# Kernel optimization log

Hardware: AMD Instinct MI355X
Metric: run time of the kernel (lower is better)

Reference implementation:

```python
import jax, jax.numpy as jnp
import numpy as np

IN_FEATURES = 4096
OUT_FEATURES = 11008
GROUP_SIZE = 32
M_TOKENS = 32
Q_MID = 8  # int4 midpoint: dequant = (q - 8) * scale + zero


def setup_inputs() -> dict:
    key = jax.random.key(0)
    k1, k2, k3, k4 = jax.random.split(key, 4)
    n_groups = IN_FEATURES // GROUP_SIZE
    inputs = {
        "input": jax.random.normal(k1, (M_TOKENS, IN_FEATURES), dtype=jnp.float32),
        "weight": jax.random.randint(k2, (OUT_FEATURES, IN_FEATURES), 0, 16, dtype=jnp.int32),
        "scales_and_zeros": jax.random.normal(k3, (n_groups, OUT_FEATURES, 2), dtype=jnp.float32),
        "bias": jax.random.normal(k4, (OUT_FEATURES,), dtype=jnp.float32),
        "group_size": GROUP_SIZE,
    }
    return inputs


def reference(input, weight, scales_and_zeros, bias, group_size):
    out_features, in_features = weight.shape
    n_groups = in_features // group_size
    # scales/zeros per (group, out) -> [out, n_groups]
    scale = scales_and_zeros[..., 0].T  # [out, G]
    zero = scales_and_zeros[..., 1].T   # [out, G]
    # dequantize int4 weight: w = (q - 8) * scale + zero, per group along in_features
    q = weight.astype(jnp.float32).reshape(out_features, n_groups, group_size)
    w_fp = (q - Q_MID) * scale[:, :, None] + zero[:, :, None]  # [out, G, gs]
    w_fp = w_fp.reshape(out_features, in_features)
    # y = x @ W^T + b
    y = jnp.einsum("bi,oi->bo", input, w_fp) + bias
    return y
```

## Files before the change

kernel.cpp:

```cpp
#include <hip/hip_runtime.h>
#include <hip/hip_bf16.h>
#include <stdint.h>

#define M_TOK 32
#define IN_F 4096
#define OUT_F 11008
#define NSPLIT 4
#define KRANGE (IN_F / NSPLIT)
#define KC 128
#define NTILE 64
#define LDA 136
#define LDB 136

typedef __attribute__((ext_vector_type(8))) short bf16x8;
typedef __attribute__((ext_vector_type(4))) float f32x4;

__device__ inline uint32_t pack_bf16(float a, float b) {
    __hip_bfloat16 ha = __float2bfloat16(a);
    __hip_bfloat16 hb = __float2bfloat16(b);
    uint16_t ua = *(uint16_t*)&ha;
    uint16_t ub = *(uint16_t*)&hb;
    return (uint32_t)ua | ((uint32_t)ub << 16);
}

__global__ void init_out_kernel(const float* __restrict__ bias, float* __restrict__ out) {
    int o = blockIdx.x * 256 + threadIdx.x;
    int m = blockIdx.y;
    out[(size_t)m * OUT_F + o] = bias[o];
}

__launch_bounds__(256)
__global__ void qgemm_kernel(const float* __restrict__ x,
                             const int* __restrict__ wq,
                             const float* __restrict__ sz,
                             float* __restrict__ out) {
    __shared__ __align__(16) short A[M_TOK * LDA];
    __shared__ __align__(16) short B[NTILE * LDB];

    const int bid = blockIdx.x;
    const int ks = bid & 3;
    const int nb = bid >> 2;
    const int o0 = nb * NTILE;
    const int k0 = ks * KRANGE;

    const int t  = threadIdx.x;
    const int w  = t >> 6;
    const int l  = t & 63;
    const int lm = l & 15;
    const int lq = l >> 4;

    f32x4 acc0 = {0.f, 0.f, 0.f, 0.f};
    f32x4 acc1 = {0.f, 0.f, 0.f, 0.f};

    for (int ch = 0; ch < KRANGE / KC; ++ch) {
        const int kb = k0 + ch * KC;

        int4  qv[8];
        float2 szv[8];
        #pragma unroll
        for (int rep = 0; rep < 8; ++rep) {
            int s   = t + rep * 256;
            int r   = s >> 5;
            int kc4 = (s & 31) << 2;
            int kg  = kb + kc4;
            qv[rep]  = *(const int4*)(wq + (size_t)(o0 + r) * IN_F + kg);
            int g    = kg >> 5;
            szv[rep] = *(const float2*)(sz + ((size_t)g * OUT_F + (o0 + r)) * 2);
        }
        float4 av[2][2];
        #pragma unroll
        for (int rep = 0; rep < 2; ++rep) {
            int slot = t + rep * 256;
            int am   = slot >> 4;
            int ak   = (slot & 15) * 8;
            const float* src = x + (size_t)am * IN_F + kb + ak;
            av[rep][0] = *(const float4*)(src);
            av[rep][1] = *(const float4*)(src + 4);
        }

        #pragma unroll
        for (int rep = 0; rep < 8; ++rep) {
            int s   = t + rep * 256;
            int r   = s >> 5;
            int kc4 = (s & 31) << 2;
            float sc = szv[rep].x, zp = szv[rep].y;
            float w0 = (float)(qv[rep].x - 8) * sc + zp;
            float w1 = (float)(qv[rep].y - 8) * sc + zp;
            float w2 = (float)(qv[rep].z - 8) * sc + zp;
            float w3 = (float)(qv[rep].w - 8) * sc + zp;
            uint2 p;
            p.x = pack_bf16(w0, w1);
            p.y = pack_bf16(w2, w3);
            *(uint2*)&B[r * LDB + kc4] = p;
        }
        #pragma unroll
        for (int rep = 0; rep < 2; ++rep) {
            int slot = t + rep * 256;
            int am   = slot >> 4;
            int ak   = (slot & 15) * 8;
            uint4 p;
            p.x = pack_bf16(av[rep][0].x, av[rep][0].y);
            p.y = pack_bf16(av[rep][0].z, av[rep][0].w);
            p.z = pack_bf16(av[rep][1].x, av[rep][1].y);
            p.w = pack_bf16(av[rep][1].z, av[rep][1].w);
            *(uint4*)&A[am * LDA + ak] = p;
        }
        __syncthreads();

        #pragma unroll
        for (int kk = 0; kk < KC / 32; ++kk) {
            bf16x8 af0 = *(const bf16x8*)&A[lm * LDA        + kk * 32 + lq * 8];
            bf16x8 af1 = *(const bf16x8*)&A[(16 + lm) * LDA + kk * 32 + lq * 8];
            bf16x8 bfr = *(const bf16x8*)&B[(w * 16 + lm) * LDB + kk * 32 + lq * 8];
            acc0 = __builtin_amdgcn_mfma_f32_16x16x32_bf16(af0, bfr, acc0, 0, 0, 0);
            acc1 = __builtin_amdgcn_mfma_f32_16x16x32_bf16(af1, bfr, acc1, 0, 0, 0);
        }
        __syncthreads();
    }

    const int ocol = o0 + w * 16 + lm;
    #pragma unroll
    for (int i = 0; i < 4; ++i) {
        int m0 = lq * 4 + i;
        atomicAdd(&out[(size_t)m0 * OUT_F + ocol], acc0[i]);
        atomicAdd(&out[(size_t)(16 + m0) * OUT_F + ocol], acc1[i]);
    }
}

extern "C" void kernel_launch(void* const* d_in, const int* in_sizes, int n_in,
                              void* d_out, int out_size, void* d_ws, size_t ws_size,
                              hipStream_t stream) {
    const float* x    = (const float*)d_in[0];
    const int*   wq   = (const int*)d_in[1];
    const float* sz   = (const float*)d_in[2];
    const float* bias = (const float*)d_in[3];
    float* out = (float*)d_out;

    dim3 gi(OUT_F / 256, M_TOK);
    init_out_kernel<<<gi, 256, 0, stream>>>(bias, out);

    dim3 gg((OUT_F / NTILE) * NSPLIT);
    qgemm_kernel<<<gg, 256, 0, stream>>>(x, wq, sz, out);
}
```

Before: 279.0 us.

## Load MFMA fragments directly from global memory, drop LDS staging, split K eight ways

Each lane now loads its weight and activation fragments straight from global memory in the MFMA operand layout and converts them in registers, so the shared-memory tiles and both __syncthreads per chunk are gone. The dequant is folded into a single FMA by precomputing zero minus 8 times scale. The K split goes from 4 to 8 to launch more blocks. The costs are redundant activation loads across waves and blocks, less coalesced 32-byte-per-lane weight reads, and twice as many atomic adds into the output.

```diff
diff --git a/kernel.cpp b/kernel.cpp
--- a/kernel.cpp
+++ b/kernel.cpp
@@ -5,12 +5,8 @@
 #define M_TOK 32
 #define IN_F 4096
 #define OUT_F 11008
-#define NSPLIT 4
+#define NSPLIT 8
 #define KRANGE (IN_F / NSPLIT)
-#define KC 128
-#define NTILE 64
-#define LDA 136
-#define LDB 136
 
 typedef __attribute__((ext_vector_type(8))) short bf16x8;
 typedef __attribute__((ext_vector_type(4))) float f32x4;
@@ -34,91 +30,62 @@
                              const int* __restrict__ wq,
                              const float* __restrict__ sz,
                              float* __restrict__ out) {
-    __shared__ __align__(16) short A[M_TOK * LDA];
-    __shared__ __align__(16) short B[NTILE * LDB];
+    const int bid = blockIdx.x;
+    const int ks  = bid & (NSPLIT - 1);
+    const int nb  = bid >> 3;
+    const int t   = threadIdx.x;
+    const int wv  = t >> 6;
+    const int l   = t & 63;
+    const int lm  = l & 15;
+    const int lq  = l >> 4;
 
-    const int bid = blockIdx.x;
-    const int ks = bid & 3;
-    const int nb = bid >> 2;
-    const int o0 = nb * NTILE;
-    const int k0 = ks * KRANGE;
+    const int row = nb * 64 + wv * 16 + lm;
+    const int k0  = ks * KRANGE;
 
-    const int t  = threadIdx.x;
-    const int w  = t >> 6;
-    const int l  = t & 63;
-    const int lm = l & 15;
-    const int lq = l >> 4;
+    const int*   wp  = wq + (size_t)row * IN_F + k0 + lq * 8;
+    const float* xp0 = x + (size_t)lm * IN_F + k0 + lq * 8;
+    const float* xp1 = xp0 + (size_t)16 * IN_F;
+    const float* szp = sz + ((size_t)(k0 >> 5) * OUT_F + row) * 2;
 
     f32x4 acc0 = {0.f, 0.f, 0.f, 0.f};
     f32x4 acc1 = {0.f, 0.f, 0.f, 0.f};
 
-    for (int ch = 0; ch < KRANGE / KC; ++ch) {
-        const int kb = k0 + ch * KC;
+    #pragma unroll 4
+    for (int s = 0; s < KRANGE / 32; ++s) {
+        int4   q0 = *(const int4*)(wp);
+        int4   q1 = *(const int4*)(wp + 4);
+        float2 sv = *(const float2*)(szp);
+        float4 xa = *(const float4*)(xp0);
+        float4 xb = *(const float4*)(xp0 + 4);
+        float4 xc = *(const float4*)(xp1);
+        float4 xd = *(const float4*)(xp1 + 4);
+        wp  += 32;
+        xp0 += 32;
+        xp1 += 32;
+        szp += (size_t)OUT_F * 2;
 
-        int4  qv[8];
-        float2 szv[8];
-        #pragma unroll
-        for (int rep = 0; rep < 8; ++rep) {
-            int s   = t + rep * 256;
-            int r   = s >> 5;
-            int kc4 = (s & 31) << 2;
-            int kg  = kb + kc4;
-            qv[rep]  = *(const int4*)(wq + (size_t)(o0 + r) * IN_F + kg);
-            int g    = kg >> 5;
-            szv[rep] = *(const float2*)(sz + ((size_t)g * OUT_F + (o0 + r)) * 2);
-        }
-        float4 av[2][2];
-        #pragma unroll
-        for (int rep = 0; rep < 2; ++rep) {
-            int slot = t + rep * 256;
-            int am   = slot >> 4;
-            int ak   = (slot & 15) * 8;
-            const float* src = x + (size_t)am * IN_F + kb + ak;
-            av[rep][0] = *(const float4*)(src);
-            av[rep][1] = *(const float4*)(src + 4);
-        }
+        const float sc = sv.x;
+        const float zp = sv.y - 8.0f * sv.x;
 
-        #pragma unroll
-        for (int rep = 0; rep < 8; ++rep) {
-            int s   = t + rep * 256;
-            int r   = s >> 5;
-            int kc4 = (s & 31) << 2;
-            float sc = szv[rep].x, zp = szv[rep].y;
-            float w0 = (float)(qv[rep].x - 8) * sc + zp;
-            float w1 = (float)(qv[rep].y - 8) * sc + zp;
-            float w2 = (float)(qv[rep].z - 8) * sc + zp;
-            float w3 = (float)(qv[rep].w - 8) * sc + zp;
-            uint2 p;
-            p.x = pack_bf16(w0, w1);
-            p.y = pack_bf16(w2, w3);
-            *(uint2*)&B[r * LDB + kc4] = p;
-        }
-        #pragma unroll
-        for (int rep = 0; rep < 2; ++rep) {
-            int slot = t + rep * 256;
-            int am   = slot >> 4;
-            int ak   = (slot & 15) * 8;
-            uint4 p;
-            p.x = pack_bf16(av[rep][0].x, av[rep][0].y);
-            p.y = pack_bf16(av[rep][0].z, av[rep][0].w);
-            p.z = pack_bf16(av[rep][1].x, av[rep][1].y);
-            p.w = pack_bf16(av[rep][1].z, av[rep][1].w);
-            *(uint4*)&A[am * LDA + ak] = p;
-        }
-        __syncthreads();
+        union { bf16x8 v; uint32_t u[4]; } bf, a0, a1;
+        bf.u[0] = pack_bf16((float)q0.x * sc + zp, (float)q0.y * sc + zp);
+        bf.u[1] = pack_bf16((float)q0.z * sc + zp, (float)q0.w * sc + zp);
+        bf.u[2] = pack_bf16((float)q1.x * sc + zp, (float)q1.y * sc + zp);
+        bf.u[3] = pack_bf16((float)q1.z * sc + zp, (float)q1.w * sc + zp);
+        a0.u[0] = pack_bf16(xa.x, xa.y);
+        a0.u[1] = pack_bf16(xa.z, xa.w);
+        a0.u[2] = pack_bf16(xb.x, xb.y);
+        a0.u[3] = pack_bf16(xb.z, xb.w);
+        a1.u[0] = pack_bf16(xc.x, xc.y);
+        a1.u[1] = pack_bf16(xc.z, xc.w);
+        a1.u[2] = pack_bf16(xd.x, xd.y);
+        a1.u[3] = pack_bf16(xd.z, xd.w);
 
-        #pragma unroll
-        for (int kk = 0; kk < KC / 32; ++kk) {
-            bf16x8 af0 = *(const bf16x8*)&A[lm * LDA        + kk * 32 + lq * 8];
-            bf16x8 af1 = *(const bf16x8*)&A[(16 + lm) * LDA + kk * 32 + lq * 8];
-            bf16x8 bfr = *(const bf16x8*)&B[(w * 16 + lm) * LDB + kk * 32 + lq * 8];
-            acc0 = __builtin_amdgcn_mfma_f32_16x16x32_bf16(af0, bfr, acc0, 0, 0, 0);
-            acc1 = __builtin_amdgcn_mfma_f32_16x16x32_bf16(af1, bfr, acc1, 0, 0, 0);
-        }
-        __syncthreads();
+        acc0 = __builtin_amdgcn_mfma_f32_16x16x32_bf16(a0.v, bf.v, acc0, 0, 0, 0);
+        acc1 = __builtin_amdgcn_mfma_f32_16x16x32_bf16(a1.v, bf.v, acc1, 0, 0, 0);
     }
 
-    const int ocol = o0 + w * 16 + lm;
+    const int ocol = nb * 64 + wv * 16 + lm;
     #pragma unroll
     for (int i = 0; i < 4; ++i) {
         int m0 = lq * 4 + i;
@@ -139,6 +106,6 @@
     dim3 gi(OUT_F / 256, M_TOK);
     init_out_kernel<<<gi, 256, 0, stream>>>(bias, out);
 
-    dim3 gg((OUT_F / NTILE) * NSPLIT);
+    dim3 gg((OUT_F / 64) * NSPLIT);
     qgemm_kernel<<<gg, 256, 0, stream>>>(x, wq, sz, out);
 }
```

After: 278.5 us. No clear change (-0.2%).
